# Performance work log

Measured on AMD Instinct MI355X. Metric: run time of the kernel, lower is better.

Reference implementation:

```python
import jax, jax.numpy as jnp
import numpy as np

B, D, H, W = 16, 384, 64, 64
Dq, Dv, NH, DFF = 768, 384, 12, 1536
EPS = 1e-5


def setup_inputs() -> dict:
    key = jax.random.key(0)
    ks = jax.random.split(key, 8)

    def w(k, out_c, in_c):
        return (jax.random.normal(k, (out_c, in_c), jnp.float32) / np.float32(np.sqrt(in_c)))

    return {
        "x": jax.random.normal(ks[0], (B, D, H, W), jnp.float32),
        "ln1_w": jnp.ones((D, H, W), jnp.float32),
        "ln1_b": jnp.zeros((D, H, W), jnp.float32),
        "qw": w(ks[1], Dq, D), "qb": jnp.zeros((Dq,), jnp.float32),
        "kw": w(ks[2], Dq, D), "kb": jnp.zeros((Dq,), jnp.float32),
        "vw": w(ks[3], Dv, D), "vb": jnp.zeros((Dv,), jnp.float32),
        "hu_w": w(ks[4], D, Dv), "hu_b": jnp.zeros((D,), jnp.float32),
        "ln2_w": jnp.ones((D, H, W), jnp.float32),
        "ln2_b": jnp.zeros((D, H, W), jnp.float32),
        "ff1_w": w(ks[5], DFF, D), "ff1_b": jnp.zeros((DFF,), jnp.float32),
        "ff2_w": w(ks[6], D, DFF), "ff2_b": jnp.zeros((D,), jnp.float32),
    }


def layernorm(x, w, b):
    # torch.nn.LayerNorm((D, H, W)): normalize over last 3 dims, biased var
    mu = x.mean(axis=(1, 2, 3), keepdims=True)
    var = x.var(axis=(1, 2, 3), keepdims=True)
    return (x - mu) * jax.lax.rsqrt(var + EPS) * w + b


def conv1x1(x, w, b):
    # 1x1 conv == channel-mixing matmul; x: (B, Cin, H, W), w: (Cout, Cin)
    return jnp.einsum('bdhw,od->bohw', x, w) + b[None, :, None, None]


def reference(x, ln1_w, ln1_b, qw, qb, kw, kb, vw, vb, hu_w, hu_b,
              ln2_w, ln2_b, ff1_w, ff1_b, ff2_w, ff2_b):
    a = layernorm(x, ln1_w, ln1_b)
    Q = conv1x1(a, qw, qb)  # (B, Dq, H, W)
    K = conv1x1(a, kw, kb)  # (B, Dq, H, W)
    V = conv1x1(a, vw, vb)  # (B, Dv, H, W)

    Q = jax.nn.softmax(Q, axis=1)  # softmax over channels (subtract-max is built in)
    K = jax.nn.softmax(K.reshape(B, Dq, H * W), axis=-1).reshape(B, Dq, H, W)

    Qh = Q.reshape(B, NH, Dq // NH, H, W)
    Kh = K.reshape(B, NH, Dq // NH, H, W)
    Vh = V.reshape(B, NH, Dv // NH, H, W)

    # kernel_size=1: adaptive_avg_pool2d(KV, 1) * 1 == spatial mean of K (x) V,
    # and the grouped 1x1 conv is a per-(batch,head) (Dv/h x Dq/h) matmul on Q.
    KV = jnp.einsum('bhqyx,bhvyx->bhqv', Kh, Vh) / np.float32(H * W)
    QKV = jnp.einsum('bhqv,bhqyx->bhvyx', KV, Qh).reshape(B, Dv, H, W)

    attn = conv1x1(QKV, hu_w, hu_b)  # head unification, (B, D, H, W)
    x = x + attn
    x = layernorm(x, ln2_w, ln2_b)
    ff = conv1x1(jax.nn.gelu(conv1x1(x, ff1_w, ff1_b), approximate=False), ff2_w, ff2_b)
    return x + ff
```

## Files before the change

kernel.cpp:

```cpp
#include <hip/hip_runtime.h>
#include <hip/hip_bf16.h>

using u16 = unsigned short;
typedef __attribute__((ext_vector_type(4))) float f32x4;
typedef __bf16 bf16x8 __attribute__((ext_vector_type(8)));
typedef short s16x4 __attribute__((ext_vector_type(4)));
typedef short s16x8 __attribute__((ext_vector_type(8)));

#define DEVI __device__ __forceinline__

DEVI float b2f(u16 u) {
    union { unsigned i; float f; } x; x.i = ((unsigned)u) << 16; return x.f;
}
DEVI u16 f2b(float f) {
    union { float f; unsigned i; } x; x.f = f;
    unsigned r = (x.i + 0x7fffu + ((x.i >> 16) & 1u)) >> 16;
    return (u16)r;
}

DEVI float gelu_fast(float v) {
    float t = v * (1.5957691f + 0.0713548162f * v * v);
    return v / (1.f + __expf(-t));
}

static constexpr long long PX = 1572864LL;
static constexpr long long PQ = 3145728LL;
static constexpr long long PH = 6291456LL;

DEVI void gl_lds16(const u16* g, u16* l) {
    __builtin_amdgcn_global_load_lds(
        (const __attribute__((address_space(1))) unsigned int*)g,
        (__attribute__((address_space(3))) unsigned int*)l, 16, 0, 0);
}

__global__ __launch_bounds__(256)
void wconv_kernel(const float* __restrict__ qw, const float* __restrict__ kw,
                  const float* __restrict__ vw, const float* __restrict__ huw,
                  const float* __restrict__ ff1w, const float* __restrict__ ff2w,
                  u16* __restrict__ wcv)
{
    int blk = blockIdx.x;
    const float* src; u16* dst; int lb;
    if      (blk < 288)  { src = qw;   dst = wcv;           lb = blk; }
    else if (blk < 576)  { src = kw;   dst = wcv + 294912;  lb = blk - 288; }
    else if (blk < 720)  { src = vw;   dst = wcv + 589824;  lb = blk - 576; }
    else if (blk < 864)  { src = huw;  dst = wcv + 737280;  lb = blk - 720; }
    else if (blk < 1440) { src = ff1w; dst = wcv + 884736;  lb = blk - 864; }
    else                 { src = ff2w; dst = wcv + 1474560; lb = blk - 1440; }
    int i = (lb * 256 + threadIdx.x) * 4;
    f32x4 v = *(const f32x4*)(src + i);
    s16x4 o;
#pragma unroll
    for (int j = 0; j < 4; ++j) o[j] = (short)f2b(v[j]);
    *(s16x4*)(dst + i) = o;
}

__global__ __launch_bounds__(512, 4)
void gemm_wide_kernel(const u16* __restrict__ A, long long strideA,
                      const u16* __restrict__ Bw,
                      const float* __restrict__ bias,
                      u16* __restrict__ C, long long strideC,
                      int K, int N, int doGelu)
{
    const int tid = threadIdx.x;
    const int lane = tid & 63;
    const int w = tid >> 6;
    const int wr = w >> 2, wc = w & 3;
    const int l15 = lane & 15, l4 = lane >> 4;
    const int bm = blockIdx.x, bn = blockIdx.y, bz = blockIdx.z;

    A += (long long)bz * strideA;
    C += (long long)bz * strideC;

    __shared__ u16 lds[128 * 64 + 256 * 64];
    u16* ldsA = lds;
    u16* ldsB = lds + 128 * 64;

    f32x4 acc[4][4] = {};

    auto stage = [&](int kt) {
#pragma unroll
        for (int i = 0; i < 2; ++i) {
            int cid = tid + i * 512;
            int row = cid >> 3, c8 = cid & 7;
            int c8s = c8 ^ (row & 7);
            gl_lds16(A + (long long)(bm * 128 + row) * K + kt + c8s * 8,
                     &ldsA[cid * 8]);
        }
#pragma unroll
        for (int i = 0; i < 4; ++i) {
            int cid = tid + i * 512;
            int row = cid >> 3, c8 = cid & 7;
            int c8s = c8 ^ (row & 7);
            gl_lds16(Bw + (long long)(bn * 256 + row) * K + kt + c8s * 8,
                     &ldsB[cid * 8]);
        }
    };

    auto compute = [&]() {
#pragma unroll
        for (int kk = 0; kk < 2; ++kk) {
            bf16x8 af[4], bfr[4];
#pragma unroll
            for (int mi = 0; mi < 4; ++mi) {
                int row = wr * 64 + mi * 16 + l15;
                int idx8 = (kk * 4 + l4) ^ (row & 7);
                af[mi] = *(const bf16x8*)&ldsA[row * 64 + idx8 * 8];
            }
#pragma unroll
            for (int ni = 0; ni < 4; ++ni) {
                int row = wc * 64 + ni * 16 + l15;
                int idx8 = (kk * 4 + l4) ^ (row & 7);
                bfr[ni] = *(const bf16x8*)&ldsB[row * 64 + idx8 * 8];
            }
#pragma unroll
            for (int mi = 0; mi < 4; ++mi)
#pragma unroll
                for (int ni = 0; ni < 4; ++ni)
                    acc[mi][ni] = __builtin_amdgcn_mfma_f32_16x16x32_bf16(af[mi], bfr[ni], acc[mi][ni], 0, 0, 0);
        }
    };

    stage(0);
    asm volatile("s_waitcnt vmcnt(0)" ::: "memory");
    __syncthreads();
    for (int kt = 64; kt < K; kt += 64) {
        compute();
        __syncthreads();
        stage(kt);
        asm volatile("s_waitcnt vmcnt(0)" ::: "memory");
        __syncthreads();
    }
    compute();

    u16* st = lds;
#pragma unroll
    for (int p = 0; p < 4; ++p) {
        int rp = p >> 1, cp = p & 1;
        __syncthreads();
        if (wr == rp && (wc >> 1) == cp) {
#pragma unroll
            for (int ni = 0; ni < 4; ++ni) {
                int colL = (wc & 1) * 64 + ni * 16 + l15;
                float bv = bias ? bias[bn * 256 + cp * 128 + colL] : 0.f;
#pragma unroll
                for (int mi = 0; mi < 4; ++mi) {
#pragma unroll
                    for (int r = 0; r < 4; ++r) {
                        float v = acc[mi][ni][r] + bv;
                        if (doGelu) v = gelu_fast(v);
                        st[(mi * 16 + l4 * 4 + r) * 136 + colL] = f2b(v);
                    }
                }
            }
        }
        __syncthreads();
        int lr = tid >> 3, q = tid & 7;
        const u16* src = st + lr * 136 + q * 16;
        u16* dst = C + (long long)(bm * 128 + rp * 64 + lr) * N + bn * 256 + cp * 128 + q * 16;
        *(s16x8*)(dst)     = *(const s16x8*)(src);
        *(s16x8*)(dst + 8) = *(const s16x8*)(src + 8);
    }
}

__global__ __launch_bounds__(256, 4)
void gemm_bt_kernel(const u16* __restrict__ A, long long strideA,
                    const u16* __restrict__ Bw, long long strideB,
                    const float* __restrict__ bias,
                    u16* __restrict__ C, long long strideC,
                    float* __restrict__ Cf,
                    const u16* __restrict__ addT, long long strideAdd,
                    int K, int N, int doGelu)
{
    const int tid = threadIdx.x;
    const int lane = tid & 63;
    const int wv = tid >> 6;
    const int wr = wv >> 1, wc = wv & 1;
    const int l15 = lane & 15, l4 = lane >> 4;
    const int bm = blockIdx.x, bn = blockIdx.y, bz = blockIdx.z;

    A  += (long long)bz * strideA;
    Bw += (long long)bz * strideB;
    if (C)    C    += (long long)bz * strideC;
    if (Cf)   Cf   += (long long)bz * strideC;
    if (addT) addT += (long long)bz * strideAdd;

    __shared__ u16 lds[2][128 * 64];

    f32x4 acc[4][4] = {};

    auto stage = [&](int kt) {
#pragma unroll
        for (int i = 0; i < 4; ++i) {
            int cid = tid + i * 256;
            int row = cid >> 3, c8 = cid & 7;
            int c8s = c8 ^ (row & 7);
            gl_lds16(A + (long long)(bm * 128 + row) * K + kt + c8s * 8,
                     &lds[0][cid * 8]);
        }
#pragma unroll
        for (int i = 0; i < 4; ++i) {
            int cid = tid + i * 256;
            int row = cid >> 3, c8 = cid & 7;
            int c8s = c8 ^ (row & 7);
            gl_lds16(Bw + (long long)(bn * 128 + row) * K + kt + c8s * 8,
                     &lds[1][cid * 8]);
        }
    };

    auto compute = [&]() {
#pragma unroll
        for (int kk = 0; kk < 2; ++kk) {
            bf16x8 af[4], bfr[4];
#pragma unroll
            for (int mi = 0; mi < 4; ++mi) {
                int row = wr * 64 + mi * 16 + l15;
                int idx8 = (kk * 4 + l4) ^ (row & 7);
                af[mi] = *(const bf16x8*)&lds[0][row * 64 + idx8 * 8];
            }
#pragma unroll
            for (int ni = 0; ni < 4; ++ni) {
                int row = wc * 64 + ni * 16 + l15;
                int idx8 = (kk * 4 + l4) ^ (row & 7);
                bfr[ni] = *(const bf16x8*)&lds[1][row * 64 + idx8 * 8];
            }
#pragma unroll
            for (int mi = 0; mi < 4; ++mi)
#pragma unroll
                for (int ni = 0; ni < 4; ++ni)
                    acc[mi][ni] = __builtin_amdgcn_mfma_f32_16x16x32_bf16(af[mi], bfr[ni], acc[mi][ni], 0, 0, 0);
        }
    };

    stage(0);
    asm volatile("s_waitcnt vmcnt(0)" ::: "memory");
    __syncthreads();
    for (int kt = 64; kt < K; kt += 64) {
        compute();
        __syncthreads();
        stage(kt);
        asm volatile("s_waitcnt vmcnt(0)" ::: "memory");
        __syncthreads();
    }
    compute();

    if (!Cf) {
        u16* st = &lds[0][0];
#pragma unroll
        for (int p = 0; p < 2; ++p) {
            __syncthreads();
            if (wr == p) {
#pragma unroll
                for (int ni = 0; ni < 4; ++ni) {
                    int colL = wc * 64 + ni * 16 + l15;
                    float bv = bias ? bias[bn * 128 + colL] : 0.f;
#pragma unroll
                    for (int mi = 0; mi < 4; ++mi) {
#pragma unroll
                        for (int r = 0; r < 4; ++r) {
                            float v = acc[mi][ni][r] + bv;
                            if (doGelu) v = gelu_fast(v);
                            st[(mi * 16 + l4 * 4 + r) * 136 + colL] = f2b(v);
                        }
                    }
                }
            }
            __syncthreads();
            int lr = tid >> 2, q = tid & 3;
            const u16* src = st + lr * 136 + q * 32;
            u16* dst = C + (long long)(bm * 128 + p * 64 + lr) * N + bn * 128 + q * 32;
#pragma unroll
            for (int j = 0; j < 4; ++j)
                *(s16x8*)(dst + j * 8) = *(const s16x8*)(src + j * 8);
        }
    } else {
        float* stf = (float*)&lds[0][0];
#pragma unroll
        for (int p = 0; p < 4; ++p) {
            __syncthreads();
            if (wc == (p >> 1)) {
#pragma unroll
                for (int nj = 0; nj < 2; ++nj) {
                    int ni = (p & 1) * 2 + nj;
                    int colL = wc * 64 + ni * 16 + l15;
                    int lc = nj * 16 + l15;
                    float bv = bias ? bias[bn * 128 + colL] : 0.f;
#pragma unroll
                    for (int mi = 0; mi < 4; ++mi) {
                        int row0 = wr * 64 + mi * 16 + l4 * 4;
#pragma unroll
                        for (int r = 0; r < 4; ++r) {
                            float v = acc[mi][ni][r] + bv
                                    + b2f(addT[(long long)(bm * 128 + row0 + r) * N + bn * 128 + colL]);
                            stf[lc * 132 + row0 + r] = v;
                        }
                    }
                }
            }
            __syncthreads();
            int lc = tid >> 3, q = tid & 7;
            float* dst = Cf + (long long)(bn * 128 + p * 32 + lc) * 4096 + bm * 128 + q * 16;
            const float* src = stf + lc * 132 + q * 16;
#pragma unroll
            for (int j = 0; j < 4; ++j)
                *(f32x4*)(dst + j * 4) = *(const f32x4*)(src + j * 4);
        }
    }
}

__global__ __launch_bounds__(256)
void stats_part_kernel(const float* __restrict__ x, float* __restrict__ part)
{
    int b = blockIdx.x, cb = blockIdx.y, t = threadIdx.x;
    const float* p = x + (long long)b * PX + (long long)cb * 49152;
    float s = 0.f, q = 0.f;
    for (int i = 0; i < 48; ++i) {
        f32x4 v = *(const f32x4*)(p + (i * 256 + t) * 4);
#pragma unroll
        for (int j = 0; j < 4; ++j) { s += v[j]; q += v[j] * v[j]; }
    }
    for (int off = 32; off; off >>= 1) { s += __shfl_down(s, off); q += __shfl_down(q, off); }
    __shared__ float rs[4], rq[4];
    if ((t & 63) == 0) { rs[t >> 6] = s; rq[t >> 6] = q; }
    __syncthreads();
    if (t == 0) {
        part[(b * 32 + cb) * 2 + 0] = rs[0] + rs[1] + rs[2] + rs[3];
        part[(b * 32 + cb) * 2 + 1] = rq[0] + rq[1] + rq[2] + rq[3];
    }
}

__global__ void stats_fin_kernel(const float* __restrict__ part, float* __restrict__ mu, float* __restrict__ rsg)
{
    int b = blockIdx.x, l = threadIdx.x;
    float s = l < 32 ? part[(b * 32 + l) * 2 + 0] : 0.f;
    float q = l < 32 ? part[(b * 32 + l) * 2 + 1] : 0.f;
    for (int off = 32; off; off >>= 1) { s += __shfl_down(s, off); q += __shfl_down(q, off); }
    if (l == 0) {
        float m = s / 1572864.f;
        float v = q / 1572864.f - m * m; v = fmaxf(v, 0.f);
        mu[b] = m; rsg[b] = rsqrtf(v + 1e-5f);
    }
}

__global__ __launch_bounds__(256)
void ln_apply_T_kernel(const float* __restrict__ src, const float* __restrict__ w, const float* __restrict__ bb,
                       const float* __restrict__ mu, const float* __restrict__ rsg, u16* __restrict__ dstT)
{
    int nt = blockIdx.x, dt = blockIdx.y, b = blockIdx.z;
    int t = threadIdx.x, tx = t & 63, ty = t >> 6;
    __shared__ float tile[64][65];
    float m = mu[b], r = rsg[b];
    const long long base = (long long)b * PX;
#pragma unroll 4
    for (int i = 0; i < 16; ++i) {
        int dy = ty + i * 4;
        int d = dt * 64 + dy, n = nt * 64 + tx;
        long long widx = (long long)d * 4096 + n;
        tile[dy][tx] = (src[base + widx] - m) * r * w[widx] + bb[widx];
    }
    __syncthreads();
#pragma unroll 4
    for (int i = 0; i < 16; ++i) {
        int ny = ty + i * 4;
        int n = nt * 64 + ny, d = dt * 64 + tx;
        dstT[base + (long long)n * 384 + d] = f2b(tile[tx][ny]);
    }
}

__global__ __launch_bounds__(256)
void softmax_rows_kernel(u16* __restrict__ QT)
{
    long long row = (long long)blockIdx.x * 4 + (threadIdx.x >> 6);
    int lane = threadIdx.x & 63;
    u16* p = QT + row * 768;
    float v[12];
#pragma unroll
    for (int g = 0; g < 3; ++g) {
        s16x4 a = *(const s16x4*)(p + g * 256 + lane * 4);
#pragma unroll
        for (int j = 0; j < 4; ++j) v[g * 4 + j] = b2f((u16)a[j]);
    }
    float m = -1e30f;
#pragma unroll
    for (int j = 0; j < 12; ++j) m = fmaxf(m, v[j]);
    for (int off = 32; off; off >>= 1) m = fmaxf(m, __shfl_xor(m, off));
    float s = 0.f;
#pragma unroll
    for (int j = 0; j < 12; ++j) { v[j] = __expf(v[j] - m); s += v[j]; }
    for (int off = 32; off; off >>= 1) s += __shfl_xor(s, off);
    float inv = 1.f / s;
#pragma unroll
    for (int g = 0; g < 3; ++g) {
        s16x4 o;
#pragma unroll
        for (int j = 0; j < 4; ++j) o[j] = (short)f2b(v[g * 4 + j] * inv);
        *(s16x4*)(p + g * 256 + lane * 4) = o;
    }
}

__global__ __launch_bounds__(256)
void kv_part_kernel(const u16* __restrict__ KT, const u16* __restrict__ VT,
                    u16* __restrict__ KVp, float* __restrict__ sp)
{
    const int ch = blockIdx.x, h = blockIdx.y, b = blockIdx.z;
    const int t = threadIdx.x;
    const int lane = t & 63, w = t >> 6;

    __shared__ u16 kraw[128 * 64];
    __shared__ u16 eKT[64 * 128];
    __shared__ u16 Vt[32 * 128];
    __shared__ float reds[4][64];

    const u16* Kp = KT + (long long)b * PQ + (long long)(ch * 128) * 768 + h * 64;
    const u16* Vp = VT + (long long)b * PX + (long long)(ch * 128) * 384 + h * 32;

#pragma unroll
    for (int pass = 0; pass < 4; ++pass) {
        int cid = t + pass * 256;
        int row = cid >> 3, c8 = cid & 7;
        gl_lds16(Kp + (long long)row * 768 + c8 * 8, kraw + cid * 8);
    }

    {
        int v0 = (t & 7) * 4;
#pragma unroll
        for (int pass = 0; pass < 4; ++pass) {
            int n = (t >> 3) + pass * 32;
            s16x4 v4 = *(const s16x4*)(Vp + (long long)n * 384 + v0);
#pragma unroll
            for (int j = 0; j < 4; ++j) {
                int row = v0 + j;
                Vt[row * 128 + (n ^ ((row & 7) << 3))] = (u16)v4[j];
            }
        }
    }

    asm volatile("s_waitcnt vmcnt(0)" ::: "memory");
    __syncthreads();

    const int c = lane;
    {
        float s = 0.f;
        const int swz = (c & 7) << 3;
#pragma unroll
        for (int r8 = 0; r8 < 4; ++r8) {
            int rbase = w * 32 + r8 * 8;
            s16x8 buf;
#pragma unroll
            for (int j = 0; j < 8; ++j) {
                float e = __expf(b2f(kraw[(rbase + j) * 64 + c]));
                s += e;
                buf[j] = (short)f2b(e);
            }
            *(s16x8*)&eKT[c * 128 + (rbase ^ swz)] = buf;
        }
        reds[w][c] = s;
    }
    __syncthreads();

    if (t < 64)
        sp[((long long)(b * 12 + h) * 32 + ch) * 64 + t] =
            reds[0][t] + reds[1][t] + reds[2][t] + reds[3][t];

    const int l15 = lane & 15, l4 = lane >> 4;
    const int qrow = w * 16 + l15;
    const int sa = (qrow & 7) << 3;
    const int v0row = l15, v1row = 16 + l15;
    const int s0 = (v0row & 7) << 3, s1 = (v1row & 7) << 3;
    f32x4 acc0 = {}, acc1 = {};
#pragma unroll
    for (int ns = 0; ns < 4; ++ns) {
        int na = ns * 32 + l4 * 8;
        bf16x8 a  = *(const bf16x8*)&eKT[qrow * 128 + (na ^ sa)];
        bf16x8 b0 = *(const bf16x8*)&Vt[v0row * 128 + (na ^ s0)];
        bf16x8 b1 = *(const bf16x8*)&Vt[v1row * 128 + (na ^ s1)];
        acc0 = __builtin_amdgcn_mfma_f32_16x16x32_bf16(a, b0, acc0, 0, 0, 0);
        acc1 = __builtin_amdgcn_mfma_f32_16x16x32_bf16(a, b1, acc1, 0, 0, 0);
    }
    u16* Kb = KVp + ((long long)(b * 12 + h) * 32 + ch) * 2048;
#pragma unroll
    for (int r = 0; r < 4; ++r) {
        int q = w * 16 + l4 * 4 + r;
        Kb[q * 32 + l15]      = f2b(acc0[r]);
        Kb[q * 32 + 16 + l15] = f2b(acc1[r]);
    }
}

__global__ __launch_bounds__(256)
void kv_fin_kernel(const u16* __restrict__ KVp, const float* __restrict__ sp,
                   u16* __restrict__ WeffT)
{
    const int h = blockIdx.x, b = blockIdx.y;
    const int t = threadIdx.x;
    __shared__ float fac[64];
    __shared__ float kvt[32][64];

    const long long pb = (long long)(b * 12 + h) * 32;
    if (t < 64) {
        float s = 0.f;
#pragma unroll
        for (int ch = 0; ch < 32; ++ch) s += sp[(pb + ch) * 64 + t];
        fac[t] = 1.f / (s * 4096.f);
    }
    __syncthreads();

    const int v0 = (t & 3) * 8, q = t >> 2;
    float acc[8] = {};
#pragma unroll
    for (int ch = 0; ch < 32; ++ch) {
        s16x8 kv8 = *(const s16x8*)&KVp[(pb + ch) * 2048 + q * 32 + v0];
#pragma unroll
        for (int j = 0; j < 8; ++j) acc[j] += b2f((u16)kv8[j]);
    }
    float fq = fac[q];
#pragma unroll
    for (int j = 0; j < 8; ++j) kvt[v0 + j][q] = acc[j] * fq;
    __syncthreads();

    u16* Wb = WeffT + (long long)b * 294912;
    for (int i = t; i < 64 * 384; i += 256) {
        int qq = i / 384, cc = i % 384;
        int cv = cc - h * 32;
        float val = (cv >= 0 && cv < 32) ? kvt[cv][qq] : 0.f;
        Wb[(long long)(h * 64 + qq) * 384 + cc] = f2b(val);
    }
}

__global__ __launch_bounds__(256)
void wtrans_kernel(const float* __restrict__ w, const float* __restrict__ bb,
                   u16* __restrict__ wT, u16* __restrict__ bT)
{
    int nt = blockIdx.x, dt = blockIdx.y;
    const float* src = blockIdx.z ? bb : w;
    u16* dst = blockIdx.z ? bT : wT;
    int t = threadIdx.x, tx = t & 63, ty = t >> 6;
    __shared__ float tile[64][65];
#pragma unroll 4
    for (int i = 0; i < 16; ++i) {
        int dy = ty + i * 4;
        tile[dy][tx] = src[(long long)(dt * 64 + dy) * 4096 + nt * 64 + tx];
    }
    __syncthreads();
#pragma unroll 4
    for (int i = 0; i < 16; ++i) {
        int ny = ty + i * 4;
        dst[(long long)(nt * 64 + ny) * 384 + dt * 64 + tx] = f2b(tile[tx][ny]);
    }
}

__global__ __launch_bounds__(256)
void resid1T_kernel(const float* __restrict__ x, const u16* __restrict__ attnT,
                    u16* __restrict__ sT, float* __restrict__ part2)
{
    int nt = blockIdx.x, dt = blockIdx.y, b = blockIdx.z;
    int t = threadIdx.x, tx = t & 63, ty = t >> 6;
    __shared__ float tile[64][65];
    const long long base = (long long)b * PX;
#pragma unroll 4
    for (int i = 0; i < 16; ++i) {
        int dy = ty + i * 4;
        tile[dy][tx] = x[base + (long long)(dt * 64 + dy) * 4096 + nt * 64 + tx];
    }
    __syncthreads();
    float ps = 0.f, pq = 0.f;
#pragma unroll 4
    for (int i = 0; i < 16; ++i) {
        int ny = ty + i * 4;
        long long idx = base + (long long)(nt * 64 + ny) * 384 + dt * 64 + tx;
        float val = tile[tx][ny] + b2f(attnT[idx]);
        sT[idx] = f2b(val);
        ps += val; pq += val * val;
    }
    for (int off = 32; off; off >>= 1) { ps += __shfl_down(ps, off); pq += __shfl_down(pq, off); }
    __shared__ float rs[4], rq[4];
    if ((t & 63) == 0) { rs[t >> 6] = ps; rq[t >> 6] = pq; }
    __syncthreads();
    if (t == 0) {
        int bid = (b * 6 + dt) * 64 + nt;
        part2[bid * 2 + 0] = rs[0] + rs[1] + rs[2] + rs[3];
        part2[bid * 2 + 1] = rq[0] + rq[1] + rq[2] + rq[3];
    }
}

__global__ __launch_bounds__(256)
void stats_fin2_kernel(const float* __restrict__ part2, float* __restrict__ mu, float* __restrict__ rsg)
{
    int b = blockIdx.x, t = threadIdx.x;
    float s = 0.f, q = 0.f;
    for (int i = t; i < 384; i += 256) { s += part2[(b * 384 + i) * 2]; q += part2[(b * 384 + i) * 2 + 1]; }
    for (int off = 32; off; off >>= 1) { s += __shfl_down(s, off); q += __shfl_down(q, off); }
    __shared__ float rs[4], rq[4];
    if ((t & 63) == 0) { rs[t >> 6] = s; rq[t >> 6] = q; }
    __syncthreads();
    if (t == 0) {
        float S = rs[0] + rs[1] + rs[2] + rs[3], Q = rq[0] + rq[1] + rq[2] + rq[3];
        float m = S / 1572864.f;
        float v = Q / 1572864.f - m * m; v = fmaxf(v, 0.f);
        mu[b] = m; rsg[b] = rsqrtf(v + 1e-5f);
    }
}

__global__ __launch_bounds__(256)
void ln2_apply_kernel(const u16* __restrict__ sT, const u16* __restrict__ wT, const u16* __restrict__ bT,
                      const float* __restrict__ mu, const float* __restrict__ rsg, u16* __restrict__ x2T)
{
    int blk = blockIdx.x, b = blockIdx.y, t = threadIdx.x;
    float m = mu[b], r = rsg[b];
    long long wi = (long long)blk * 2048 + t * 8;
    long long gi = (long long)b * PX + wi;
    s16x8 sv = *(const s16x8*)(sT + gi);
    s16x8 wv = *(const s16x8*)(wT + wi);
    s16x8 bv = *(const s16x8*)(bT + wi);
    s16x8 o;
#pragma unroll
    for (int j = 0; j < 8; ++j)
        o[j] = (short)f2b((b2f((u16)sv[j]) - m) * r * b2f((u16)wv[j]) + b2f((u16)bv[j]));
    *(s16x8*)(x2T + gi) = o;
}

extern "C" void kernel_launch(void* const* d_in, const int* in_sizes, int n_in,
                              void* d_out, int out_size, void* d_ws, size_t ws_size,
                              hipStream_t stream)
{
    const float* x    = (const float*)d_in[0];
    const float* ln1w = (const float*)d_in[1];
    const float* ln1b = (const float*)d_in[2];
    const float* qw   = (const float*)d_in[3];
    const float* qb   = (const float*)d_in[4];
    const float* kw   = (const float*)d_in[5];
    const float* kb   = (const float*)d_in[6];
    const float* vw   = (const float*)d_in[7];
    const float* vb   = (const float*)d_in[8];
    const float* huw  = (const float*)d_in[9];
    const float* hub  = (const float*)d_in[10];
    const float* ln2w = (const float*)d_in[11];
    const float* ln2b = (const float*)d_in[12];
    const float* ff1w = (const float*)d_in[13];
    const float* ff1b = (const float*)d_in[14];
    const float* ff2w = (const float*)d_in[15];
    const float* ff2b = (const float*)d_in[16];
    float* out = (float*)d_out;

    char* ws = (char*)d_ws;
    u16*   aT    = (u16*)(ws + 0);
    u16*   QT    = (u16*)(ws + 50331648LL);
    u16*   KT    = (u16*)(ws + 150994944LL);
    u16*   VT    = (u16*)(ws + 251658240LL);
    u16*   WeffT = (u16*)(ws + 301989888LL);
    u16*   wcv   = (u16*)(ws + 311427072LL);
    float* fbuf  = (float*)(ws + 315555840LL);

    u16*   KVp    = (u16*)(ws + 0);
    float* sp     = (float*)(ws + 25165824LL);
    u16*   WcombB = (u16*)(ws + 27525120LL);

    u16* sT = KT;
    u16* wT = (u16*)(ws + 150994944LL + 50331648LL);
    u16* bT = (u16*)(ws + 150994944LL + 53477376LL);
    u16* g8 = KT;

    u16* x2T   = QT;
    u16* attnT = VT;

    u16* qwB   = wcv;
    u16* kwB   = wcv + 294912;
    u16* vwB   = wcv + 589824;
    u16* huwB  = wcv + 737280;
    u16* ff1wB = wcv + 884736;
    u16* ff2wB = wcv + 1474560;

    float* part1 = fbuf;
    float* mu1   = fbuf + 1024;
    float* rs1   = fbuf + 1040;
    float* part2 = fbuf + 1056;
    float* mu2   = part2 + 12288;
    float* rs2   = mu2 + 16;

    wconv_kernel<<<2016, 256, 0, stream>>>(qw, kw, vw, huw, ff1w, ff2w, wcv);

    stats_part_kernel<<<dim3(16, 32), 256, 0, stream>>>(x, part1);
    stats_fin_kernel<<<16, 64, 0, stream>>>(part1, mu1, rs1);
    ln_apply_T_kernel<<<dim3(64, 6, 16), 256, 0, stream>>>(x, ln1w, ln1b, mu1, rs1, aT);

    gemm_wide_kernel<<<dim3(32, 3, 16), 512, 0, stream>>>(aT, PX, qwB, qb, QT, PQ, 384, 768, 0);
    gemm_wide_kernel<<<dim3(32, 3, 16), 512, 0, stream>>>(aT, PX, kwB, kb, KT, PQ, 384, 768, 0);
    gemm_bt_kernel<<<dim3(32, 3, 16), 256, 0, stream>>>(aT, PX, vwB, 0, vb, VT, PX, nullptr, nullptr, 0, 384, 384, 0);

    softmax_rows_kernel<<<16384, 256, 0, stream>>>(QT);

    kv_part_kernel<<<dim3(32, 12, 16), 256, 0, stream>>>(KT, VT, KVp, sp);
    kv_fin_kernel<<<dim3(12, 16), 256, 0, stream>>>(KVp, sp, WeffT);

    wtrans_kernel<<<dim3(64, 6, 2), 256, 0, stream>>>(ln2w, ln2b, wT, bT);

    gemm_bt_kernel<<<dim3(3, 6, 16), 256, 0, stream>>>(huwB, 0, WeffT, 294912, nullptr, WcombB, 294912, nullptr, nullptr, 0, 384, 768, 0);

    gemm_bt_kernel<<<dim3(32, 3, 16), 256, 0, stream>>>(QT, PQ, WcombB, 294912, hub, attnT, PX, nullptr, nullptr, 0, 768, 384, 0);

    resid1T_kernel<<<dim3(64, 6, 16), 256, 0, stream>>>(x, attnT, sT, part2);
    stats_fin2_kernel<<<16, 256, 0, stream>>>(part2, mu2, rs2);
    ln2_apply_kernel<<<dim3(768, 16), 256, 0, stream>>>(sT, wT, bT, mu2, rs2, x2T);

    for (int c = 0; c < 2; ++c) {
        gemm_wide_kernel<<<dim3(32, 6, 8), 512, 0, stream>>>(
            x2T + (long long)c * 8 * PX, PX, ff1wB, ff1b,
            g8, PH, 384, 1536, 1);
        gemm_bt_kernel<<<dim3(32, 3, 8), 256, 0, stream>>>(
            g8, PH, ff2wB, 0, ff2b,
            nullptr, PX, out + (long long)c * 8 * PX,
            x2T + (long long)c * 8 * PX, PX, 1536, 384, 0);
    }
}
```

Baseline: 807.3 us.

## Fuse Q/K/V projections into one GEMM launch and drop wide-tile GEMM

```diff
diff --git a/kernel.cpp b/kernel.cpp
--- a/kernel.cpp
+++ b/kernel.cpp
@@ -55,45 +55,56 @@
     *(s16x4*)(dst + i) = o;
 }
 
-__global__ __launch_bounds__(512, 4)
-void gemm_wide_kernel(const u16* __restrict__ A, long long strideA,
-                      const u16* __restrict__ Bw,
-                      const float* __restrict__ bias,
-                      u16* __restrict__ C, long long strideC,
-                      int K, int N, int doGelu)
+__global__ __launch_bounds__(256)
+void bcat_kernel(const float* __restrict__ qb, const float* __restrict__ kb,
+                 const float* __restrict__ vb, float* __restrict__ o)
+{
+    int i = blockIdx.x * 256 + threadIdx.x;
+    if (i < 768)       o[i] = qb[i];
+    else if (i < 1536) o[i] = kb[i - 768];
+    else if (i < 1920) o[i] = vb[i - 1536];
+}
+
+__global__ __launch_bounds__(256, 4)
+void gemm_qkv_kernel(const u16* __restrict__ A, long long strideA,
+                     const u16* __restrict__ Bw,
+                     const float* __restrict__ bias,
+                     u16* __restrict__ Q, u16* __restrict__ Kd, u16* __restrict__ V,
+                     int K)
 {
     const int tid = threadIdx.x;
     const int lane = tid & 63;
-    const int w = tid >> 6;
-    const int wr = w >> 2, wc = w & 3;
+    const int wv = tid >> 6;
+    const int wr = wv >> 1, wc = wv & 1;
     const int l15 = lane & 15, l4 = lane >> 4;
     const int bm = blockIdx.x, bn = blockIdx.y, bz = blockIdx.z;
 
     A += (long long)bz * strideA;
-    C += (long long)bz * strideC;
-
-    __shared__ u16 lds[128 * 64 + 256 * 64];
-    u16* ldsA = lds;
-    u16* ldsB = lds + 128 * 64;
+    u16* dstBase; int Nout; int colBase;
+    if (bn < 6)       { dstBase = Q  + (long long)bz * PQ; Nout = 768; colBase = bn * 128; }
+    else if (bn < 12) { dstBase = Kd + (long long)bz * PQ; Nout = 768; colBase = (bn - 6) * 128; }
+    else              { dstBase = V  + (long long)bz * PX; Nout = 384; colBase = (bn - 12) * 128; }
+
+    __shared__ u16 lds[2][128 * 64];
 
     f32x4 acc[4][4] = {};
 
     auto stage = [&](int kt) {
 #pragma unroll
-        for (int i = 0; i < 2; ++i) {
-            int cid = tid + i * 512;
+        for (int i = 0; i < 4; ++i) {
+            int cid = tid + i * 256;
             int row = cid >> 3, c8 = cid & 7;
             int c8s = c8 ^ (row & 7);
             gl_lds16(A + (long long)(bm * 128 + row) * K + kt + c8s * 8,
-                     &ldsA[cid * 8]);
+                     &lds[0][cid * 8]);
         }
 #pragma unroll
         for (int i = 0; i < 4; ++i) {
-            int cid = tid + i * 512;
+            int cid = tid + i * 256;
             int row = cid >> 3, c8 = cid & 7;
             int c8s = c8 ^ (row & 7);
-            gl_lds16(Bw + (long long)(bn * 256 + row) * K + kt + c8s * 8,
-                     &ldsB[cid * 8]);
+            gl_lds16(Bw + (long long)(bn * 128 + row) * K + kt + c8s * 8,
+                     &lds[1][cid * 8]);
         }
     };
 
@@ -105,13 +116,13 @@
             for (int mi = 0; mi < 4; ++mi) {
                 int row = wr * 64 + mi * 16 + l15;
                 int idx8 = (kk * 4 + l4) ^ (row & 7);
-                af[mi] = *(const bf16x8*)&ldsA[row * 64 + idx8 * 8];
+                af[mi] = *(const bf16x8*)&lds[0][row * 64 + idx8 * 8];
             }
 #pragma unroll
             for (int ni = 0; ni < 4; ++ni) {
                 int row = wc * 64 + ni * 16 + l15;
                 int idx8 = (kk * 4 + l4) ^ (row & 7);
-                bfr[ni] = *(const bf16x8*)&ldsB[row * 64 + idx8 * 8];
+                bfr[ni] = *(const bf16x8*)&lds[1][row * 64 + idx8 * 8];
             }
 #pragma unroll
             for (int mi = 0; mi < 4; ++mi)
@@ -133,33 +144,30 @@
     }
     compute();
 
-    u16* st = lds;
-#pragma unroll
-    for (int p = 0; p < 4; ++p) {
-        int rp = p >> 1, cp = p & 1;
+    u16* st = &lds[0][0];
+#pragma unroll
+    for (int p = 0; p < 2; ++p) {
         __syncthreads();
-        if (wr == rp && (wc >> 1) == cp) {
+        if (wr == p) {
 #pragma unroll
             for (int ni = 0; ni < 4; ++ni) {
-                int colL = (wc & 1) * 64 + ni * 16 + l15;
-                float bv = bias ? bias[bn * 256 + cp * 128 + colL] : 0.f;
+                int colL = wc * 64 + ni * 16 + l15;
+                float bv = bias[bn * 128 + colL];
 #pragma unroll
                 for (int mi = 0; mi < 4; ++mi) {
 #pragma unroll
-                    for (int r = 0; r < 4; ++r) {
-                        float v = acc[mi][ni][r] + bv;
-                        if (doGelu) v = gelu_fast(v);
-                        st[(mi * 16 + l4 * 4 + r) * 136 + colL] = f2b(v);
-                    }
+                    for (int r = 0; r < 4; ++r)
+                        st[(mi * 16 + l4 * 4 + r) * 136 + colL] = f2b(acc[mi][ni][r] + bv);
                 }
             }
         }
         __syncthreads();
-        int lr = tid >> 3, q = tid & 7;
-        const u16* src = st + lr * 136 + q * 16;
-        u16* dst = C + (long long)(bm * 128 + rp * 64 + lr) * N + bn * 256 + cp * 128 + q * 16;
-        *(s16x8*)(dst)     = *(const s16x8*)(src);
-        *(s16x8*)(dst + 8) = *(const s16x8*)(src + 8);
+        int lr = tid >> 2, q = tid & 3;
+        const u16* src = st + lr * 136 + q * 32;
+        u16* dst = dstBase + (long long)(bm * 128 + p * 64 + lr) * Nout + colBase + q * 32;
+#pragma unroll
+        for (int j = 0; j < 4; ++j)
+            *(s16x8*)(dst + j * 8) = *(const s16x8*)(src + j * 8);
     }
 }
 
@@ -663,11 +671,9 @@
     u16* attnT = VT;
 
     u16* qwB   = wcv;
-    u16* kwB   = wcv + 294912;
-    u16* vwB   = wcv + 589824;
-    u16* huwB  = wcv + 737280;
     u16* ff1wB = wcv + 884736;
     u16* ff2wB = wcv + 1474560;
+    u16* huwB  = wcv + 737280;
 
     float* part1 = fbuf;
     float* mu1   = fbuf + 1024;
@@ -675,16 +681,16 @@
     float* part2 = fbuf + 1056;
     float* mu2   = part2 + 12288;
     float* rs2   = mu2 + 16;
+    float* qkvb  = rs2 + 16;
 
     wconv_kernel<<<2016, 256, 0, stream>>>(qw, kw, vw, huw, ff1w, ff2w, wcv);
+    bcat_kernel<<<8, 256, 0, stream>>>(qb, kb, vb, qkvb);
 
     stats_part_kernel<<<dim3(16, 32), 256, 0, stream>>>(x, part1);
     stats_fin_kernel<<<16, 64, 0, stream>>>(part1, mu1, rs1);
     ln_apply_T_kernel<<<dim3(64, 6, 16), 256, 0, stream>>>(x, ln1w, ln1b, mu1, rs1, aT);
 
-    gemm_wide_kernel<<<dim3(32, 3, 16), 512, 0, stream>>>(aT, PX, qwB, qb, QT, PQ, 384, 768, 0);
-    gemm_wide_kernel<<<dim3(32, 3, 16), 512, 0, stream>>>(aT, PX, kwB, kb, KT, PQ, 384, 768, 0);
-    gemm_bt_kernel<<<dim3(32, 3, 16), 256, 0, stream>>>(aT, PX, vwB, 0, vb, VT, PX, nullptr, nullptr, 0, 384, 384, 0);
+    gemm_qkv_kernel<<<dim3(32, 15, 16), 256, 0, stream>>>(aT, PX, qwB, qkvb, QT, KT, VT, 384);
 
     softmax_rows_kernel<<<16384, 256, 0, stream>>>(QT);
 
@@ -702,9 +708,9 @@
     ln2_apply_kernel<<<dim3(768, 16), 256, 0, stream>>>(sT, wT, bT, mu2, rs2, x2T);
 
     for (int c = 0; c < 2; ++c) {
-        gemm_wide_kernel<<<dim3(32, 6, 8), 512, 0, stream>>>(
-            x2T + (long long)c * 8 * PX, PX, ff1wB, ff1b,
-            g8, PH, 384, 1536, 1);
+        gemm_bt_kernel<<<dim3(32, 12, 8), 256, 0, stream>>>(
+            x2T + (long long)c * 8 * PX, PX, ff1wB, 0, ff1b,
+            g8, PH, nullptr, nullptr, 0, 384, 1536, 1);
         gemm_bt_kernel<<<dim3(32, 3, 8), 256, 0, stream>>>(
             g8, PH, ff2wB, 0, ff2b,
             nullptr, PX, out + (long long)c * 8 * PX,
```

Result: faster. 759.4 us (-5.9%).
